# Optimization experiments

Hardware: AMD Instinct MI355X
Metric: run time of the kernel (lower is better)

Reference implementation:

```python
import jax, jax.numpy as jnp
import numpy as np

NH = 10      # number of nearest source neighbors per target (init arg nh)
EPS = 1e-10  # numerical guard for inverse-distance weights


def setup_inputs() -> dict:
    key = jax.random.key(0)
    k1, k2 = jax.random.split(key)
    # x: [B, N_source, C] field values at source points
    x = jax.random.normal(k1, (8, 4096, 8), dtype=jnp.float32)
    # rel: [N_target, N_source, 2] relative (lon, lat) offsets target->source
    rel = jax.random.normal(k2, (16384, 4096, 2), dtype=jnp.float32)
    return {"x": x, "rel": rel}


def reference(x, rel):
    # input_dropout has p=0 -> identity, so it is omitted.
    # Pairwise Euclidean distances: [N_target, N_source]
    d = jnp.sqrt(jnp.sum(rel * rel, axis=-1))
    # nh nearest sources per target (top_k of negated distances)
    neg_topd, idx = jax.lax.top_k(-d, NH)          # idx: [T, NH]
    dist = -neg_topd                               # [T, NH]
    # inverse-distance weights, normalized over the NH neighbors
    w = 1.0 / (dist + EPS)
    w = w / jnp.sum(w, axis=-1, keepdims=True)     # [T, NH]
    # gather neighbor values: [B, T, NH, C]
    vals = jnp.take(x, idx, axis=1)
    # weighted sum over neighbors -> [B, T, C]
    return jnp.einsum('tk,btkc->btc', w, vals)
```

## Files before the change

kernel.cpp:

```cpp
#include <hip/hip_runtime.h>

#define NH 10
#define NB 8
#define NC 8
#define NT 16384
#define NS 4096
#define EPSW 1e-10f
#define FINF 3.402823466e+38f

typedef float float4n __attribute__((ext_vector_type(4)));

__device__ __forceinline__ void insert1(float t, int ti, float v[NH], int id[NH]) {
    bool c[NH];
#pragma unroll
    for (int k = 0; k < NH; ++k) c[k] = t < v[k];
    float nv[NH]; int ni[NH];
    nv[0] = c[0] ? t : v[0];
    ni[0] = c[0] ? ti : id[0];
#pragma unroll
    for (int k = 1; k < NH; ++k) {
        nv[k] = __builtin_amdgcn_fmed3f(t, v[k - 1], v[k]);
        ni[k] = c[k - 1] ? id[k - 1] : (c[k] ? ti : id[k]);
    }
#pragma unroll
    for (int k = 0; k < NH; ++k) { v[k] = nv[k]; id[k] = ni[k]; }
}

__global__ __launch_bounds__(256) void knn_interp_kernel(
    const float* __restrict__ x,
    const float* __restrict__ rel,
    float* __restrict__ out)
{
    const int lane = threadIdx.x & 63;
    const int wave = threadIdx.x >> 6;
    const int t = blockIdx.x * 4 + wave;

    float v[NH];
    int   id[NH];
#pragma unroll
    for (int k = 0; k < NH; ++k) { v[k] = FINF; id[k] = 0x7FFFFFFF; }

    const float4n* relrow = (const float4n*)(rel + (size_t)t * (NS * 2));

    float4n cur[4];
#pragma unroll
    for (int u = 0; u < 4; ++u)
        cur[u] = __builtin_nontemporal_load(&relrow[u * 64 + lane]);

#pragma unroll 1
    for (int j = 0; j < 7; ++j) {
        float4n nxt[4];
#pragma unroll
        for (int u = 0; u < 4; ++u)
            nxt[u] = __builtin_nontemporal_load(&relrow[(j + 1) * 256 + u * 64 + lane]);
#pragma unroll
        for (int u = 0; u < 4; ++u) {
            const int f4i = j * 256 + u * 64 + lane;
            float d2a = cur[u].x * cur[u].x + cur[u].y * cur[u].y;
            float d2b = cur[u].z * cur[u].z + cur[u].w * cur[u].w;
            insert1(d2a, f4i * 2,     v, id);
            insert1(d2b, f4i * 2 + 1, v, id);
        }
#pragma unroll
        for (int u = 0; u < 4; ++u) cur[u] = nxt[u];
    }
#pragma unroll
    for (int u = 0; u < 4; ++u) {
        const int f4i = 7 * 256 + u * 64 + lane;
        float d2a = cur[u].x * cur[u].x + cur[u].y * cur[u].y;
        float d2b = cur[u].z * cur[u].z + cur[u].w * cur[u].w;
        insert1(d2a, f4i * 2,     v, id);
        insert1(d2b, f4i * 2 + 1, v, id);
    }

    float rd[NH];
    int   ridx[NH];
#pragma unroll
    for (int r = 0; r < NH; ++r) {
        unsigned long long key =
            ((unsigned long long)__float_as_uint(v[0]) << 32) | (unsigned)id[0];
        unsigned long long m = key;
#pragma unroll
        for (int o = 32; o > 0; o >>= 1) {
            unsigned long long other = __shfl_xor(m, o, 64);
            m = (other < m) ? other : m;
        }
        rd[r]   = __uint_as_float((unsigned)(m >> 32));
        ridx[r] = (int)(unsigned)(m & 0xFFFFFFFFull);

        bool won = (key == m);
#pragma unroll
        for (int k = 0; k < NH - 1; ++k) {
            v[k]  = won ? v[k + 1]  : v[k];
            id[k] = won ? id[k + 1] : id[k];
        }
        v[NH - 1]  = won ? FINF : v[NH - 1];
        id[NH - 1] = won ? 0x7FFFFFFF : id[NH - 1];
    }

    float w[NH];
    float wsum = 0.f;
#pragma unroll
    for (int r = 0; r < NH; ++r) {
        float d = sqrtf(rd[r]);
        w[r] = 1.0f / (d + EPSW);
        wsum += w[r];
    }
    const float inv = 1.0f / wsum;

    const int b = lane >> 3;
    const int c = lane & 7;
    const float* xb = x + ((size_t)b * NS) * NC + c;
    float acc = 0.f;
#pragma unroll
    for (int r = 0; r < NH; ++r) {
        acc += w[r] * xb[(size_t)ridx[r] * NC];
    }
    out[((size_t)b * NT + t) * NC + c] = acc * inv;
}

extern "C" void kernel_launch(void* const* d_in, const int* in_sizes, int n_in,
                              void* d_out, int out_size, void* d_ws, size_t ws_size,
                              hipStream_t stream) {
    const float* x   = (const float*)d_in[0];
    const float* rel = (const float*)d_in[1];
    float* out = (float*)d_out;

    dim3 grid(NT / 4);
    dim3 block(256);
    knn_interp_kernel<<<grid, block, 0, stream>>>(x, rel, out);
}
```

Measured before the change: 661.8 us.

## Filter kNN candidates by distance threshold with ballot compaction before top-k

Instead of inserting every source distance into a per-lane sorted top-10 list, each lane tests against a fixed squared-distance threshold and passing candidates are compacted via ballot/popcount into a per-wave shared buffer. The top-k insertion then runs only over the compacted candidates using packed 64-bit distance/index keys. If too few or too many candidates pass, the kernel rescans the whole row exactly. This aims to remove the per-element sorting-network cost that dominates the scan, at the expense of a threshold tuned to the expected distance distribution and a slow fallback path.

New measurement: 651.9 us. No clear change (-1.5%).

```diff
diff --git a/kernel.cpp b/kernel.cpp
--- a/kernel.cpp
+++ b/kernel.cpp
@@ -6,24 +6,22 @@
 #define NT 16384
 #define NS 4096
 #define EPSW 1e-10f
-#define FINF 3.402823466e+38f
+#define CAP 256
+#define T2  0.02f
 
 typedef float float4n __attribute__((ext_vector_type(4)));
 
-__device__ __forceinline__ void insert1(float t, int ti, float v[NH], int id[NH]) {
+__device__ __forceinline__ void insert_key(unsigned long long key, unsigned long long kv[NH]) {
     bool c[NH];
 #pragma unroll
-    for (int k = 0; k < NH; ++k) c[k] = t < v[k];
-    float nv[NH]; int ni[NH];
-    nv[0] = c[0] ? t : v[0];
-    ni[0] = c[0] ? ti : id[0];
+    for (int k = 0; k < NH; ++k) c[k] = key < kv[k];
+    unsigned long long nv[NH];
+    nv[0] = c[0] ? key : kv[0];
 #pragma unroll
-    for (int k = 1; k < NH; ++k) {
-        nv[k] = __builtin_amdgcn_fmed3f(t, v[k - 1], v[k]);
-        ni[k] = c[k - 1] ? id[k - 1] : (c[k] ? ti : id[k]);
-    }
+    for (int k = 1; k < NH; ++k)
+        nv[k] = c[k] ? (c[k - 1] ? kv[k - 1] : key) : kv[k];
 #pragma unroll
-    for (int k = 0; k < NH; ++k) { v[k] = nv[k]; id[k] = ni[k]; }
+    for (int k = 0; k < NH; ++k) kv[k] = nv[k];
 }
 
 __global__ __launch_bounds__(256) void knn_interp_kernel(
@@ -35,12 +33,25 @@
     const int wave = threadIdx.x >> 6;
     const int t = blockIdx.x * 4 + wave;
 
-    float v[NH];
-    int   id[NH];
-#pragma unroll
-    for (int k = 0; k < NH; ++k) { v[k] = FINF; id[k] = 0x7FFFFFFF; }
+    __shared__ unsigned long long cbuf[4][CAP];
+    unsigned long long* cb = cbuf[wave];
+    const unsigned long long lmask = (1ull << lane) - 1ull;
 
     const float4n* relrow = (const float4n*)(rel + (size_t)t * (NS * 2));
+
+    int cnt = 0;
+
+    auto scan2 = [&](float d2, int ix) {
+        unsigned long long m = __ballot(d2 < T2);
+        if (m) {
+            if (d2 < T2) {
+                int pos = cnt + (int)__popcll(m & lmask);
+                if (pos < CAP)
+                    cb[pos] = ((unsigned long long)__float_as_uint(d2) << 32) | (unsigned)ix;
+            }
+            cnt += (int)__popcll(m);
+        }
+    };
 
     float4n cur[4];
 #pragma unroll
@@ -58,8 +69,8 @@
             const int f4i = j * 256 + u * 64 + lane;
             float d2a = cur[u].x * cur[u].x + cur[u].y * cur[u].y;
             float d2b = cur[u].z * cur[u].z + cur[u].w * cur[u].w;
-            insert1(d2a, f4i * 2,     v, id);
-            insert1(d2b, f4i * 2 + 1, v, id);
+            scan2(d2a, f4i * 2);
+            scan2(d2b, f4i * 2 + 1);
         }
 #pragma unroll
         for (int u = 0; u < 4; ++u) cur[u] = nxt[u];
@@ -69,17 +80,34 @@
         const int f4i = 7 * 256 + u * 64 + lane;
         float d2a = cur[u].x * cur[u].x + cur[u].y * cur[u].y;
         float d2b = cur[u].z * cur[u].z + cur[u].w * cur[u].w;
-        insert1(d2a, f4i * 2,     v, id);
-        insert1(d2b, f4i * 2 + 1, v, id);
+        scan2(d2a, f4i * 2);
+        scan2(d2b, f4i * 2 + 1);
+    }
+
+    __syncthreads();
+
+    unsigned long long kv[NH];
+#pragma unroll
+    for (int k = 0; k < NH; ++k) kv[k] = ~0ull;
+
+    if (cnt >= NH && cnt <= CAP) {
+        for (int i = lane; i < cnt; i += 64)
+            insert_key(cb[i], kv);
+    } else {
+        for (int f = lane; f < NS / 2; f += 64) {
+            float4n q = relrow[f];
+            float d2a = q.x * q.x + q.y * q.y;
+            float d2b = q.z * q.z + q.w * q.w;
+            insert_key(((unsigned long long)__float_as_uint(d2a) << 32) | (unsigned)(2 * f),     kv);
+            insert_key(((unsigned long long)__float_as_uint(d2b) << 32) | (unsigned)(2 * f + 1), kv);
+        }
     }
 
     float rd[NH];
     int   ridx[NH];
 #pragma unroll
     for (int r = 0; r < NH; ++r) {
-        unsigned long long key =
-            ((unsigned long long)__float_as_uint(v[0]) << 32) | (unsigned)id[0];
-        unsigned long long m = key;
+        unsigned long long m = kv[0];
 #pragma unroll
         for (int o = 32; o > 0; o >>= 1) {
             unsigned long long other = __shfl_xor(m, o, 64);
@@ -87,15 +115,10 @@
         }
         rd[r]   = __uint_as_float((unsigned)(m >> 32));
         ridx[r] = (int)(unsigned)(m & 0xFFFFFFFFull);
-
-        bool won = (key == m);
+        bool won = (kv[0] == m);
 #pragma unroll
-        for (int k = 0; k < NH - 1; ++k) {
-            v[k]  = won ? v[k + 1]  : v[k];
-            id[k] = won ? id[k + 1] : id[k];
-        }
-        v[NH - 1]  = won ? FINF : v[NH - 1];
-        id[NH - 1] = won ? 0x7FFFFFFF : id[NH - 1];
+        for (int k = 0; k < NH - 1; ++k) kv[k] = won ? kv[k + 1] : kv[k];
+        kv[NH - 1] = won ? ~0ull : kv[NH - 1];
     }
 
     float w[NH];
```
